# Optimization experiments

Measured on AMD Instinct MI355X. Metric: run time of the kernel, lower is better.

## Reference

```python
import jax, jax.numpy as jnp
import numpy as np

DECAY = 0.99
EPS = 1e-05
B, C, H, W = 64, 64, 64, 64   # C == embedding_dim
K = 512                       # num_embedding


def setup_inputs() -> dict:
    key = jax.random.key(0)
    k1, k2 = jax.random.split(key)
    inp = jax.random.normal(k1, (B, C, H, W), dtype=jnp.float32)
    embedding = jax.random.normal(k2, (C, K), dtype=jnp.float32)
    cluster_size = jnp.zeros((K,), dtype=jnp.float32)
    embedding_avg = embedding  # buffer initialized as a clone of embedding
    return {"input": inp, "embedding": embedding,
            "cluster_size": cluster_size, "embedding_avg": embedding_avg}


def reference(input, embedding, cluster_size, embedding_avg):
    # NCHW -> NHWC, flatten to [N, C]
    x = jnp.transpose(input, (0, 2, 3, 1))           # [B,H,W,C]
    flat = x.reshape(-1, embedding.shape[0])          # [N,C]
    # squared L2 distances to all K codes: [N,K]
    dist = (jnp.sum(flat * flat, axis=1, keepdims=True)
            - 2.0 * flat @ embedding
            + jnp.sum(embedding * embedding, axis=0, keepdims=True))
    ind = jnp.argmin(dist, axis=1)                    # [N] int
    # gather codes (uses OLD embedding, as in torch)
    quantize = jnp.take(embedding.T, ind, axis=0).reshape(x.shape)  # [B,H,W,C]
    # EMA updates (training branch). Avoid materializing one-hot:
    counts = jnp.zeros((K,), dtype=flat.dtype).at[ind].add(1.0)      # onehot.sum(0)
    embedding_sum = jax.ops.segment_sum(flat, ind, num_segments=K).T  # [C,K] == flat.T @ onehot
    new_cluster_size = cluster_size * DECAY + (1.0 - DECAY) * counts
    new_embedding_avg = embedding_avg * DECAY + (1.0 - DECAY) * embedding_sum
    n = jnp.sum(new_cluster_size)
    cs = (new_cluster_size + EPS) / (n + K * EPS) * n
    new_embedding = new_embedding_avg / cs[None, :]
    # commitment loss and straight-through estimator
    diff = jnp.mean((jax.lax.stop_gradient(quantize) - x) ** 2)
    quantize_st = x + jax.lax.stop_gradient(quantize - x)
    out = jnp.transpose(quantize_st, (0, 3, 1, 2))    # back to NCHW
    embedding_ind = ind.reshape(x.shape[:-1])         # [B,H,W]
    return out, diff, embedding_ind, new_embedding, new_cluster_size, new_embedding_avg
```

## Files before the change

kernel.cpp:

```cpp
#include <hip/hip_runtime.h>
#include <cstdint>
#include <cstddef>

typedef _Float16 half4v __attribute__((ext_vector_type(4)));
typedef _Float16 half8v __attribute__((ext_vector_type(8)));
typedef float    f32x4  __attribute__((ext_vector_type(4)));

#define N_PTS   262144
#define CDIM    64
#define KCODES  512
#define TAUA    5e-3f
#define FLAG_CAP 65536u

#define OFF_DIFF 16777216u
#define OFF_IND  16777217u
#define OFF_EMB  17039361u
#define OFF_CSZ  17072129u
#define OFF_AVG  17072641u

__global__ __launch_bounds__(512) void k_main(
    const float* __restrict__ in, const float* __restrict__ emb,
    float* __restrict__ out,
    int* __restrict__ ind_buf, float* __restrict__ diff_acc,
    unsigned* __restrict__ nflag, int* __restrict__ flaglist)
{
    __shared__ __align__(16) char bsm[133120];
    float* ee2_lds = (float*)(bsm + 131072);
    const int tid = threadIdx.x;

    {
        const int col = tid;
        const int xr  = (col & 7) << 4;
        float s = 0.f;
        #pragma unroll
        for (int c0 = 0; c0 < CDIM; c0 += 4) {
            float v[4];
            #pragma unroll
            for (int i = 0; i < 4; ++i) v[i] = emb[(c0 + i)*KCODES + col];
            half4v h, lo;
            #pragma unroll
            for (int i = 0; i < 4; ++i) {
                s = fmaf(v[i], v[i], s);
                _Float16 hh = (_Float16)v[i];
                h[i]  = hh;
                lo[i] = (_Float16)(v[i] - (float)hh);
            }
            const int wb = col*128 + ((c0*2) ^ xr);
            *(half4v*)(bsm + wb)         = h;
            *(half4v*)(bsm + 65536 + wb) = lo;
        }
        ee2_lds[col] = 0.5f * s;
    }
    __syncthreads();

    const int w  = tid >> 6, l = tid & 63;
    const int g  = l >> 4,  lc = l & 15;

    for (int r = 0; r < 2; ++r) {
        const int pbase = (blockIdx.x << 10) + (r << 9) + (w << 6);
        const int b     = pbase >> 12;
        const float* inb = in + ((size_t)b << 18) + ((pbase & 4095) + lc);

        half8v ah[4][2], al[4][2];
        float xs = 0.f;
        #pragma unroll
        for (int t = 0; t < 4; ++t)
            #pragma unroll
            for (int s = 0; s < 2; ++s)
                #pragma unroll
                for (int j = 0; j < 8; ++j) {
                    const int c = s*32 + g*8 + j;
                    const float x = inb[(size_t)c*4096 + t*16];
                    xs = fmaf(x, x, xs);
                    const float xf = -x;
                    const _Float16 hh = (_Float16)xf;
                    ah[t][s][j] = hh;
                    al[t][s][j] = (_Float16)(xf - (float)hh);
                }

        float d1[4][4], d2[4][4]; int k1[4][4];
        #pragma unroll
        for (int t = 0; t < 4; ++t)
            #pragma unroll
            for (int rr = 0; rr < 4; ++rr) { d1[t][rr] = 3.4e38f; d2[t][rr] = 3.4e38f; k1[t][rr] = 0; }

        for (int ct = 0; ct < 32; ++ct) {
            const int col  = (ct << 4) + lc;
            const float sd = ee2_lds[col];
            const int rb   = col*128 + ((g*16) ^ ((col & 7) << 4));
            half8v bh0 = *(const half8v*)(bsm + rb);
            half8v bh1 = *(const half8v*)(bsm + (rb ^ 64));
            half8v bl0 = *(const half8v*)(bsm + 65536 + rb);
            half8v bl1 = *(const half8v*)(bsm + 65536 + (rb ^ 64));

            #pragma unroll
            for (int t = 0; t < 4; ++t) {
                f32x4 acc0 = {sd, sd, sd, sd};
                f32x4 acc1 = {0.f, 0.f, 0.f, 0.f};
                acc0 = __builtin_amdgcn_mfma_f32_16x16x32_f16(al[t][0], bh0, acc0, 0, 0, 0);
                acc1 = __builtin_amdgcn_mfma_f32_16x16x32_f16(al[t][1], bh1, acc1, 0, 0, 0);
                acc0 = __builtin_amdgcn_mfma_f32_16x16x32_f16(ah[t][0], bl0, acc0, 0, 0, 0);
                acc1 = __builtin_amdgcn_mfma_f32_16x16x32_f16(ah[t][1], bl1, acc1, 0, 0, 0);
                acc0 = __builtin_amdgcn_mfma_f32_16x16x32_f16(ah[t][0], bh0, acc0, 0, 0, 0);
                acc1 = __builtin_amdgcn_mfma_f32_16x16x32_f16(ah[t][1], bh1, acc1, 0, 0, 0);
                #pragma unroll
                for (int rr = 0; rr < 4; ++rr) {
                    const float d = acc0[rr] + acc1[rr];
                    const bool cc = d < d1[t][rr];
                    d2[t][rr] = fminf(d2[t][rr], fmaxf(d, d1[t][rr]));
                    d1[t][rr] = fminf(d1[t][rr], d);
                    k1[t][rr] = cc ? col : k1[t][rr];
                }
            }
        }

        #pragma unroll
        for (int m = 1; m <= 8; m <<= 1) {
            #pragma unroll
            for (int t = 0; t < 4; ++t)
                #pragma unroll
                for (int rr = 0; rr < 4; ++rr) {
                    const float od1 = __shfl_xor(d1[t][rr], m);
                    const int   ok1 = __shfl_xor(k1[t][rr], m);
                    const float od2 = __shfl_xor(d2[t][rr], m);
                    const float nd2 = fminf(fmaxf(d1[t][rr], od1), fminf(d2[t][rr], od2));
                    const bool take = (od1 < d1[t][rr]) || (od1 == d1[t][rr] && ok1 < k1[t][rr]);
                    d1[t][rr] = take ? od1 : d1[t][rr];
                    k1[t][rr] = take ? ok1 : k1[t][rr];
                    d2[t][rr] = nd2;
                }
        }

        float ds = 0.f;
        if (lc == 0) {
            #pragma unroll
            for (int t = 0; t < 4; ++t) {
                const int nb = pbase + t*16 + (g << 2);
                int4 iv = make_int4(k1[t][0], k1[t][1], k1[t][2], k1[t][3]);
                *(int4*)(ind_buf + nb) = iv;
                #pragma unroll
                for (int rr = 0; rr < 4; ++rr) {
                    out[OFF_IND + nb + rr] = (float)k1[t][rr];
                    ds += d1[t][rr];
                    if (d2[t][rr] - d1[t][rr] < TAUA) {
                        unsigned ix = atomicAdd(nflag, 1u);
                        if (ix < FLAG_CAP) flaglist[ix] = nb + rr;
                    }
                }
            }
        }
        #pragma unroll
        for (int m = 1; m < 64; m <<= 1) {
            ds += __shfl_xor(ds, m);
            xs += __shfl_xor(xs, m);
        }
        if (l == 0) atomicAdd(diff_acc, 2.f*ds + xs);
    }
}

__global__ void k_refine(const float* __restrict__ in, const float* __restrict__ emb,
                         const unsigned* __restrict__ nflag, const int* __restrict__ flaglist,
                         int* __restrict__ ind_buf, float* __restrict__ out)
{
    const int gtid = blockIdx.x*blockDim.x + threadIdx.x;
    const int wid  = gtid >> 6;
    const int lane = threadIdx.x & 63;
    const int nw   = (gridDim.x * blockDim.x) >> 6;
    unsigned nf = *nflag; if (nf > FLAG_CAP) nf = FLAG_CAP;
    for (unsigned f = wid; f < nf; f += nw) {
        const int n = flaglist[f];
        const int b = n >> 12, hw = n & 4095;
        const float* xb = in + ((size_t)b << 18) + hw;
        const float* er = emb + lane*8;
        double dd[8] = {0,0,0,0,0,0,0,0};
        for (int c = 0; c < CDIM; ++c) {
            const double xv = (double)xb[(size_t)c << 12];
            #pragma unroll
            for (int j = 0; j < 8; ++j) {
                double t = xv - (double)er[c*KCODES + j];
                dd[j] = fma(t, t, dd[j]);
            }
        }
        double bd = 1e300; int bk = 0;
        #pragma unroll
        for (int j = 0; j < 8; ++j) {
            const int kk = lane*8 + j;
            if (dd[j] < bd) { bd = dd[j]; bk = kk; }
        }
        for (int off = 32; off; off >>= 1) {
            double od = __shfl_xor(bd, off);
            int    ok = __shfl_xor(bk, off);
            if (od < bd || (od == bd && ok < bk)) { bd = od; bk = ok; }
        }
        if (lane == 0) { ind_buf[n] = bk; out[OFF_IND + n] = (float)bk; }
    }
}

__global__ __launch_bounds__(512) void k_stats(const float* __restrict__ in,
    const int* __restrict__ ind_buf, float* __restrict__ p_sum, float* __restrict__ p_cnt)
{
    __shared__ __align__(16) char xsm[2][CDIM*128];
    __shared__ int   ind_lds[2][32];
    __shared__ float s_cnt[KCODES];

    const int tid = threadIdx.x;
    const int wg  = blockIdx.x;
    const int n0  = wg << 10;
    const int b   = n0 >> 12;
    const float* inb = in + ((size_t)b << 18) + (n0 & 4095);

    for (int i = tid; i < KCODES; i += 512) s_cnt[i] = 0.f;

    const int sc  = tid >> 3;
    const int sp  = (tid & 7) << 2;
    const int sxr = (sc & 7) << 4;
    const int wb_hi = sc*128 + ((sp*2) ^ sxr);

    const int w  = tid >> 6, l = tid & 63;
    const int g  = l >> 4,  lc = l & 15;
    const int k0w = w << 6;

    f32x4 acc[4][4];
    #pragma unroll
    for (int ci = 0; ci < 4; ++ci)
        #pragma unroll
        for (int kt = 0; kt < 4; ++kt) acc[ci][kt] = (f32x4){0.f, 0.f, 0.f, 0.f};

    {
        const float4 xv = *(const float4*)(inb + (size_t)sc*4096 + sp);
        half4v h;
        #pragma unroll
        for (int i = 0; i < 4; ++i) h[i] = (_Float16)(((const float*)&xv)[i]);
        *(half4v*)(&xsm[0][0] + wb_hi) = h;
        if (tid < 8) *(int4*)&ind_lds[0][tid*4] = *(const int4*)(ind_buf + n0 + tid*4);
    }

    for (int t = 0; t < 32; ++t) {
        __syncthreads();
        float4 nxt; int4 niv;
        if (t < 31) {
            nxt = *(const float4*)(inb + (size_t)sc*4096 + (t+1)*32 + sp);
            if (tid < 8) niv = *(const int4*)(ind_buf + n0 + (t+1)*32 + tid*4);
        }
        if (tid < 32) atomicAdd(&s_cnt[ind_lds[t & 1][tid]], 1.f);

        const char* xb = &xsm[t & 1][0];
        half8v ah[4];
        #pragma unroll
        for (int ci = 0; ci < 4; ++ci) {
            const int c  = (ci << 4) + lc;
            const int xr = (c & 7) << 4;
            ah[ci] = *(const half8v*)(xb + c*128 + ((g*16) ^ xr));
        }
        int idv[8];
        *(int4*)&idv[0] = *(const int4*)&ind_lds[t & 1][g*8];
        *(int4*)&idv[4] = *(const int4*)&ind_lds[t & 1][g*8 + 4];
        #pragma unroll
        for (int kt = 0; kt < 4; ++kt) {
            const int tgt = k0w + (kt << 4) + lc;
            half8v bf;
            #pragma unroll
            for (int j = 0; j < 8; ++j) bf[j] = (idv[j] == tgt) ? (_Float16)1.0f : (_Float16)0.0f;
            #pragma unroll
            for (int ci = 0; ci < 4; ++ci)
                acc[ci][kt] = __builtin_amdgcn_mfma_f32_16x16x32_f16(ah[ci], bf, acc[ci][kt], 0, 0, 0);
        }
        if (t < 31) {
            half4v h;
            #pragma unroll
            for (int i = 0; i < 4; ++i) h[i] = (_Float16)(((const float*)&nxt)[i]);
            *(half4v*)(&xsm[(t+1) & 1][0] + wb_hi) = h;
            if (tid < 8) *(int4*)&ind_lds[(t+1) & 1][tid*4] = niv;
        }
    }
    __syncthreads();

    float* ps = p_sum + (size_t)wg * (CDIM*KCODES);
    #pragma unroll
    for (int ci = 0; ci < 4; ++ci)
        #pragma unroll
        for (int kt = 0; kt < 4; ++kt)
            #pragma unroll
            for (int rr = 0; rr < 4; ++rr)
                ps[((ci << 4) + (g << 2) + rr)*KCODES + k0w + (kt << 4) + lc] = acc[ci][kt][rr];
    float* pc = p_cnt + wg * KCODES;
    for (int i = tid; i < KCODES; i += 512) pc[i] = s_cnt[i];
}

__global__ __launch_bounds__(256) void k_reduce1(const float* __restrict__ p_sum,
    const float* __restrict__ p_cnt, float* __restrict__ partial8,
    float* __restrict__ cnt8, int wsl)
{
    const int ic = blockIdx.x & 31, ws = blockIdx.x >> 5;
    const int i4 = ic*1024 + threadIdx.x*4;
    const float* base = p_sum + (size_t)ws*wsl*(CDIM*KCODES) + i4;
    float4 s = make_float4(0.f, 0.f, 0.f, 0.f);
    for (int w = 0; w < wsl; ++w) {
        const float4 v = *(const float4*)(base + (size_t)w*(CDIM*KCODES));
        s.x += v.x; s.y += v.y; s.z += v.z; s.w += v.w;
    }
    *(float4*)(partial8 + ws*(CDIM*KCODES) + i4) = s;
    if (ic == 0) {
        for (int k = threadIdx.x; k < KCODES; k += 256) {
            float c = 0.f;
            for (int w = 0; w < wsl; ++w) c += p_cnt[(ws*wsl + w)*KCODES + k];
            cnt8[ws*KCODES + k] = c;
        }
    }
}

__global__ __launch_bounds__(512) void k_final(const float* __restrict__ partial8,
    const float* __restrict__ cnt8, const float* __restrict__ csz,
    const float* __restrict__ eavg, const float* __restrict__ diff_acc,
    float* __restrict__ out)
{
    __shared__ float red[512];
    __shared__ float cs_lds[512];
    const int k = threadIdx.x;
    float c = 0.f;
    #pragma unroll
    for (int p = 0; p < 8; ++p) c += cnt8[p*KCODES + k];
    const float ncs = csz[k]*0.99f + 0.01f*c;
    if (blockIdx.x == 0) out[OFF_CSZ + k] = ncs;
    red[k] = ncs;
    __syncthreads();
    for (int s = 256; s > 0; s >>= 1) { if (k < s) red[k] += red[k+s]; __syncthreads(); }
    const float n = red[0];
    cs_lds[k] = (ncs + 1e-5f) / (n + 0.00512f) * n;
    if (blockIdx.x == 0 && k == 0) out[OFF_DIFF] = diff_acc[0] * (1.f/16777216.f);
    __syncthreads();
    if (k < 256) {
        const int i = (blockIdx.x*256 + k)*4;
        float4 s4 = make_float4(0.f, 0.f, 0.f, 0.f);
        #pragma unroll
        for (int p = 0; p < 8; ++p) {
            const float4 v = *(const float4*)(partial8 + p*(CDIM*KCODES) + i);
            s4.x += v.x; s4.y += v.y; s4.z += v.z; s4.w += v.w;
        }
        const float4 ea = *(const float4*)(eavg + i);
        const float a0 = ea.x*0.99f + 0.01f*s4.x;
        const float a1 = ea.y*0.99f + 0.01f*s4.y;
        const float a2 = ea.z*0.99f + 0.01f*s4.z;
        const float a3 = ea.w*0.99f + 0.01f*s4.w;
        const int kb = i & (KCODES-1);
        out[OFF_AVG + i]     = a0;  out[OFF_AVG + i + 1] = a1;
        out[OFF_AVG + i + 2] = a2;  out[OFF_AVG + i + 3] = a3;
        out[OFF_EMB + i]     = a0 / cs_lds[kb];
        out[OFF_EMB + i + 1] = a1 / cs_lds[kb + 1];
        out[OFF_EMB + i + 2] = a2 / cs_lds[kb + 2];
        out[OFF_EMB + i + 3] = a3 / cs_lds[kb + 3];
    }
}

__global__ void k_quant(const float* __restrict__ emb, const int* __restrict__ ind_buf,
                        float* __restrict__ out)
{
    const int gid = blockIdx.x*blockDim.x + threadIdx.x;
    const int i  = gid << 2;
    const int hw = i & 4095;
    const int c  = (i >> 12) & 63;
    const int b  = i >> 18;
    const int n  = (b << 12) + hw;
    const int4 iv = *(const int4*)(ind_buf + n);
    const float* er = emb + (c << 9);
    float4 o = make_float4(er[iv.x], er[iv.y], er[iv.z], er[iv.w]);
    *(float4*)(out + i) = o;
}

extern "C" void kernel_launch(void* const* d_in, const int* in_sizes, int n_in,
                              void* d_out, int out_size, void* d_ws, size_t ws_size,
                              hipStream_t stream)
{
    const float* in   = (const float*)d_in[0];
    const float* emb  = (const float*)d_in[1];
    const float* csz  = (const float*)d_in[2];
    const float* eavg = (const float*)d_in[3];
    float* out = (float*)d_out;
    char* ws = (char*)d_ws;

    int*      ind      = (int*)(ws + 2048);
    float*    diff_acc = (float*)(ws + 1050624);
    unsigned* nflag    = (unsigned*)(ws + 1050640);
    int*      flaglist = (int*)(ws + 1050656);
    const size_t off_part = 1447968;
    const int swgs = 256;
    float* p_sum    = (float*)(ws + off_part);
    float* p_cnt    = (float*)(ws + off_part + (size_t)swgs*(CDIM*KCODES)*4);
    float* partial8 = (float*)(ws + off_part + (size_t)swgs*133120);
    float* cnt8     = (float*)(ws + off_part + (size_t)swgs*133120 + 1048576);

    hipMemsetAsync(ws + 1050624, 0, 32, stream);

    hipLaunchKernelGGL(k_main,    dim3(256),   dim3(512), 0, stream, in, emb, out, ind, diff_acc, nflag, flaglist);
    hipLaunchKernelGGL(k_refine,  dim3(256),   dim3(256), 0, stream, in, emb, nflag, flaglist, ind, out);
    hipLaunchKernelGGL(k_quant,   dim3(16384), dim3(256), 0, stream, emb, ind, out);
    hipLaunchKernelGGL(k_stats,   dim3(256),   dim3(512), 0, stream, in, ind, p_sum, p_cnt);
    hipLaunchKernelGGL(k_reduce1, dim3(256),   dim3(256), 0, stream, p_sum, p_cnt, partial8, cnt8, swgs >> 3);
    hipLaunchKernelGGL(k_final,   dim3(32),    dim3(512), 0, stream, partial8, cnt8, csz, eavg, diff_acc, out);
}
```

Baseline: 209.5 us.

## Use single fp16 MFMA for distances, widen refine threshold, halve LDS

Drops the split hi/lo fp16 emulation of fp32 in the distance GEMM, so each distance tile needs 2 MFMAs instead of 6 and only one fp16 codebook copy sits in LDS. The smaller LDS footprint lets the grid double to 512 blocks with one 512-point pass each, which should raise occupancy. To compensate for the lower precision, the near-tie threshold is raised and the flag list capacity doubled, so more points go to the exact fp64 refine pass. The risk is that refine work grows a lot, or that the list overflows its cap and leaves some argmins wrong.

```diff
diff --git a/kernel.cpp b/kernel.cpp
--- a/kernel.cpp
+++ b/kernel.cpp
@@ -9,8 +9,8 @@
 #define N_PTS   262144
 #define CDIM    64
 #define KCODES  512
-#define TAUA    5e-3f
-#define FLAG_CAP 65536u
+#define TAUA    0.06f
+#define FLAG_CAP 131072u
 
 #define OFF_DIFF 16777216u
 #define OFF_IND  16777217u
@@ -24,8 +24,8 @@
     int* __restrict__ ind_buf, float* __restrict__ diff_acc,
     unsigned* __restrict__ nflag, int* __restrict__ flaglist)
 {
-    __shared__ __align__(16) char bsm[133120];
-    float* ee2_lds = (float*)(bsm + 131072);
+    __shared__ __align__(16) char bsm[65536];
+    __shared__ float ee2_lds[KCODES];
     const int tid = threadIdx.x;
 
     {
@@ -37,17 +37,13 @@
             float v[4];
             #pragma unroll
             for (int i = 0; i < 4; ++i) v[i] = emb[(c0 + i)*KCODES + col];
-            half4v h, lo;
+            half4v h;
             #pragma unroll
             for (int i = 0; i < 4; ++i) {
                 s = fmaf(v[i], v[i], s);
-                _Float16 hh = (_Float16)v[i];
-                h[i]  = hh;
-                lo[i] = (_Float16)(v[i] - (float)hh);
-            }
-            const int wb = col*128 + ((c0*2) ^ xr);
-            *(half4v*)(bsm + wb)         = h;
-            *(half4v*)(bsm + 65536 + wb) = lo;
+                h[i] = (_Float16)v[i];
+            }
+            *(half4v*)(bsm + col*128 + ((c0*2) ^ xr)) = h;
         }
         ee2_lds[col] = 0.5f * s;
     }
@@ -56,106 +52,94 @@
     const int w  = tid >> 6, l = tid & 63;
     const int g  = l >> 4,  lc = l & 15;
 
-    for (int r = 0; r < 2; ++r) {
-        const int pbase = (blockIdx.x << 10) + (r << 9) + (w << 6);
-        const int b     = pbase >> 12;
-        const float* inb = in + ((size_t)b << 18) + ((pbase & 4095) + lc);
-
-        half8v ah[4][2], al[4][2];
-        float xs = 0.f;
+    const int pbase = (blockIdx.x << 9) + (w << 6);
+    const int b     = pbase >> 12;
+    const float* inb = in + ((size_t)b << 18) + ((pbase & 4095) + lc);
+
+    half8v ah[4][2];
+    float xs = 0.f;
+    #pragma unroll
+    for (int t = 0; t < 4; ++t)
+        #pragma unroll
+        for (int s = 0; s < 2; ++s)
+            #pragma unroll
+            for (int j = 0; j < 8; ++j) {
+                const int c = s*32 + g*8 + j;
+                const float x = inb[(size_t)c*4096 + t*16];
+                xs = fmaf(x, x, xs);
+                ah[t][s][j] = (_Float16)(-x);
+            }
+
+    float d1[4][4], d2[4][4]; int k1[4][4];
+    #pragma unroll
+    for (int t = 0; t < 4; ++t)
+        #pragma unroll
+        for (int rr = 0; rr < 4; ++rr) { d1[t][rr] = 3.4e38f; d2[t][rr] = 3.4e38f; k1[t][rr] = 0; }
+
+    for (int ct = 0; ct < 32; ++ct) {
+        const int col  = (ct << 4) + lc;
+        const float sd = ee2_lds[col];
+        const int rb   = col*128 + ((g*16) ^ ((col & 7) << 4));
+        half8v bh0 = *(const half8v*)(bsm + rb);
+        half8v bh1 = *(const half8v*)(bsm + (rb ^ 64));
+
+        #pragma unroll
+        for (int t = 0; t < 4; ++t) {
+            f32x4 acc = {sd, sd, sd, sd};
+            acc = __builtin_amdgcn_mfma_f32_16x16x32_f16(ah[t][0], bh0, acc, 0, 0, 0);
+            acc = __builtin_amdgcn_mfma_f32_16x16x32_f16(ah[t][1], bh1, acc, 0, 0, 0);
+            #pragma unroll
+            for (int rr = 0; rr < 4; ++rr) {
+                const float d = acc[rr];
+                const bool cc = d < d1[t][rr];
+                d2[t][rr] = fminf(d2[t][rr], fmaxf(d, d1[t][rr]));
+                d1[t][rr] = fminf(d1[t][rr], d);
+                k1[t][rr] = cc ? col : k1[t][rr];
+            }
+        }
+    }
+
+    #pragma unroll
+    for (int m = 1; m <= 8; m <<= 1) {
         #pragma unroll
         for (int t = 0; t < 4; ++t)
             #pragma unroll
-            for (int s = 0; s < 2; ++s)
-                #pragma unroll
-                for (int j = 0; j < 8; ++j) {
-                    const int c = s*32 + g*8 + j;
-                    const float x = inb[(size_t)c*4096 + t*16];
-                    xs = fmaf(x, x, xs);
-                    const float xf = -x;
-                    const _Float16 hh = (_Float16)xf;
-                    ah[t][s][j] = hh;
-                    al[t][s][j] = (_Float16)(xf - (float)hh);
+            for (int rr = 0; rr < 4; ++rr) {
+                const float od1 = __shfl_xor(d1[t][rr], m);
+                const int   ok1 = __shfl_xor(k1[t][rr], m);
+                const float od2 = __shfl_xor(d2[t][rr], m);
+                const float nd2 = fminf(fmaxf(d1[t][rr], od1), fminf(d2[t][rr], od2));
+                const bool take = (od1 < d1[t][rr]) || (od1 == d1[t][rr] && ok1 < k1[t][rr]);
+                d1[t][rr] = take ? od1 : d1[t][rr];
+                k1[t][rr] = take ? ok1 : k1[t][rr];
+                d2[t][rr] = nd2;
+            }
+    }
+
+    float ds = 0.f;
+    if (lc == 0) {
+        #pragma unroll
+        for (int t = 0; t < 4; ++t) {
+            const int nb = pbase + t*16 + (g << 2);
+            int4 iv = make_int4(k1[t][0], k1[t][1], k1[t][2], k1[t][3]);
+            *(int4*)(ind_buf + nb) = iv;
+            #pragma unroll
+            for (int rr = 0; rr < 4; ++rr) {
+                out[OFF_IND + nb + rr] = (float)k1[t][rr];
+                ds += d1[t][rr];
+                if (d2[t][rr] - d1[t][rr] < TAUA) {
+                    unsigned ix = atomicAdd(nflag, 1u);
+                    if (ix < FLAG_CAP) flaglist[ix] = nb + rr;
                 }
-
-        float d1[4][4], d2[4][4]; int k1[4][4];
-        #pragma unroll
-        for (int t = 0; t < 4; ++t)
-            #pragma unroll
-            for (int rr = 0; rr < 4; ++rr) { d1[t][rr] = 3.4e38f; d2[t][rr] = 3.4e38f; k1[t][rr] = 0; }
-
-        for (int ct = 0; ct < 32; ++ct) {
-            const int col  = (ct << 4) + lc;
-            const float sd = ee2_lds[col];
-            const int rb   = col*128 + ((g*16) ^ ((col & 7) << 4));
-            half8v bh0 = *(const half8v*)(bsm + rb);
-            half8v bh1 = *(const half8v*)(bsm + (rb ^ 64));
-            half8v bl0 = *(const half8v*)(bsm + 65536 + rb);
-            half8v bl1 = *(const half8v*)(bsm + 65536 + (rb ^ 64));
-
-            #pragma unroll
-            for (int t = 0; t < 4; ++t) {
-                f32x4 acc0 = {sd, sd, sd, sd};
-                f32x4 acc1 = {0.f, 0.f, 0.f, 0.f};
-                acc0 = __builtin_amdgcn_mfma_f32_16x16x32_f16(al[t][0], bh0, acc0, 0, 0, 0);
-                acc1 = __builtin_amdgcn_mfma_f32_16x16x32_f16(al[t][1], bh1, acc1, 0, 0, 0);
-                acc0 = __builtin_amdgcn_mfma_f32_16x16x32_f16(ah[t][0], bl0, acc0, 0, 0, 0);
-                acc1 = __builtin_amdgcn_mfma_f32_16x16x32_f16(ah[t][1], bl1, acc1, 0, 0, 0);
-                acc0 = __builtin_amdgcn_mfma_f32_16x16x32_f16(ah[t][0], bh0, acc0, 0, 0, 0);
-                acc1 = __builtin_amdgcn_mfma_f32_16x16x32_f16(ah[t][1], bh1, acc1, 0, 0, 0);
-                #pragma unroll
-                for (int rr = 0; rr < 4; ++rr) {
-                    const float d = acc0[rr] + acc1[rr];
-                    const bool cc = d < d1[t][rr];
-                    d2[t][rr] = fminf(d2[t][rr], fmaxf(d, d1[t][rr]));
-                    d1[t][rr] = fminf(d1[t][rr], d);
-                    k1[t][rr] = cc ? col : k1[t][rr];
-                }
-            }
-        }
-
-        #pragma unroll
-        for (int m = 1; m <= 8; m <<= 1) {
-            #pragma unroll
-            for (int t = 0; t < 4; ++t)
-                #pragma unroll
-                for (int rr = 0; rr < 4; ++rr) {
-                    const float od1 = __shfl_xor(d1[t][rr], m);
-                    const int   ok1 = __shfl_xor(k1[t][rr], m);
-                    const float od2 = __shfl_xor(d2[t][rr], m);
-                    const float nd2 = fminf(fmaxf(d1[t][rr], od1), fminf(d2[t][rr], od2));
-                    const bool take = (od1 < d1[t][rr]) || (od1 == d1[t][rr] && ok1 < k1[t][rr]);
-                    d1[t][rr] = take ? od1 : d1[t][rr];
-                    k1[t][rr] = take ? ok1 : k1[t][rr];
-                    d2[t][rr] = nd2;
-                }
-        }
-
-        float ds = 0.f;
-        if (lc == 0) {
-            #pragma unroll
-            for (int t = 0; t < 4; ++t) {
-                const int nb = pbase + t*16 + (g << 2);
-                int4 iv = make_int4(k1[t][0], k1[t][1], k1[t][2], k1[t][3]);
-                *(int4*)(ind_buf + nb) = iv;
-                #pragma unroll
-                for (int rr = 0; rr < 4; ++rr) {
-                    out[OFF_IND + nb + rr] = (float)k1[t][rr];
-                    ds += d1[t][rr];
-                    if (d2[t][rr] - d1[t][rr] < TAUA) {
-                        unsigned ix = atomicAdd(nflag, 1u);
-                        if (ix < FLAG_CAP) flaglist[ix] = nb + rr;
-                    }
-                }
-            }
-        }
-        #pragma unroll
-        for (int m = 1; m < 64; m <<= 1) {
-            ds += __shfl_xor(ds, m);
-            xs += __shfl_xor(xs, m);
-        }
-        if (l == 0) atomicAdd(diff_acc, 2.f*ds + xs);
-    }
+            }
+        }
+    }
+    #pragma unroll
+    for (int m = 1; m < 64; m <<= 1) {
+        ds += __shfl_xor(ds, m);
+        xs += __shfl_xor(xs, m);
+    }
+    if (l == 0) atomicAdd(diff_acc, 2.f*ds + xs);
 }
 
 __global__ void k_refine(const float* __restrict__ in, const float* __restrict__ emb,
@@ -382,7 +366,7 @@
     float*    diff_acc = (float*)(ws + 1050624);
     unsigned* nflag    = (unsigned*)(ws + 1050640);
     int*      flaglist = (int*)(ws + 1050656);
-    const size_t off_part = 1447968;
+    const size_t off_part = 1574944;
     const int swgs = 256;
     float* p_sum    = (float*)(ws + off_part);
     float* p_cnt    = (float*)(ws + off_part + (size_t)swgs*(CDIM*KCODES)*4);
@@ -391,7 +375,7 @@
 
     hipMemsetAsync(ws + 1050624, 0, 32, stream);
 
-    hipLaunchKernelGGL(k_main,    dim3(256),   dim3(512), 0, stream, in, emb, out, ind, diff_acc, nflag, flaglist);
+    hipLaunchKernelGGL(k_main,    dim3(512),   dim3(512), 0, stream, in, emb, out, ind, diff_acc, nflag, flaglist);
     hipLaunchKernelGGL(k_refine,  dim3(256),   dim3(256), 0, stream, in, emb, nflag, flaglist, ind, out);
     hipLaunchKernelGGL(k_quant,   dim3(16384), dim3(256), 0, stream, emb, ind, out);
     hipLaunchKernelGGL(k_stats,   dim3(256),   dim3(512), 0, stream, in, ind, p_sum, p_cnt);
```

Result: slower. 342.6 us (+63.5%).
